# Optimization experiments

Measured on AMD Instinct MI355X. Metric: run time of the kernel, lower is better.

The kernel has to match this reference:

```python
import jax, jax.numpy as jnp
import numpy as np

H_PARAM = 3.0   # filtering strength h
TWS = 5         # template window size
SWS = 11        # search window size


def _shift_stack(x, window_size):
    # [N,C,H,W] -> [N,C,H,W,window_size**2] of circularly shifted copies.
    # Shift order matches the torch module: outer loop x_shift, inner y_shift,
    # roll shifts=(y_shift, x_shift) on dims (H, W).
    r = window_size // 2
    return jnp.stack(
        [jnp.roll(x, (ys, xs), axis=(2, 3))
         for xs in range(-r, r + 1) for ys in range(-r, r + 1)],
        axis=-1,
    )


def _box_filter(x, window_size):
    # Circular box-sum over H,W dims. The torch double roll loop is separable,
    # so do it as two 1-D roll sums (10 rolls instead of 25 for tws=5).
    r = window_size // 2
    s = x
    acc = x
    for k in range(1, r + 1):
        acc = acc + jnp.roll(s, k, axis=3) + jnp.roll(s, -k, axis=3)
    s2 = acc
    for k in range(1, r + 1):
        acc = acc + jnp.roll(s2, k, axis=2) + jnp.roll(s2, -k, axis=2)
    return acc


def setup_inputs() -> dict:
    key = jax.random.key(0)
    x = jax.random.uniform(key, (2, 3, 512, 512), dtype=jnp.float32)
    return {"x": x}


def reference(x):
    # luminance (RGB input: C == 3)
    xc = jnp.clip(x, 0.0, 1.0)
    y = 0.299 * xc[:, :1] + 0.587 * xc[:, 1:2] + 0.114 * xc[:, 2:3]  # [N,1,H,W]

    x_stack = _shift_stack(x, SWS)  # [N,3,H,W,sws^2]
    y_stack = _shift_stack(y, SWS)  # [N,1,H,W,sws^2]

    d2 = _box_filter((y[..., None] - y_stack) ** 2, TWS)  # [N,1,H,W,sws^2]
    distances = jnp.sqrt(d2)
    weights = jnp.exp(-distances / H_PARAM)                # [N,1,H,W,sws^2]

    denoised = (weights * x_stack).sum(axis=-1) / weights.sum(axis=-1)
    return jnp.clip(denoised, 0.0, 1.0)
```

## Files before the change

### kernel.cpp

```cpp
#include <hip/hip_runtime.h>
#include <math.h>


#define H_IMG 512
#define W_IMG 512
#define MASK  511
#define HWSZ  (H_IMG * W_IMG)
#define TILE  32
#define HALO  7
#define XD    46
#define YSTR  48
#define HSTR  44
#define VSTR  44

typedef _Float16 h2 __attribute__((ext_vector_type(2)));

__device__ __forceinline__ float fdot2(h2 a, h2 b, float c) {
#if __has_builtin(__builtin_amdgcn_fdot2)
    return __builtin_amdgcn_fdot2(a, b, c, false);
#else
    return c + (float)a.x * (float)b.x + (float)a.y * (float)b.y;
#endif
}

__device__ __forceinline__ float fast_exp2(float x) {
#if __has_builtin(__builtin_amdgcn_exp2f)
    return __builtin_amdgcn_exp2f(x);
#else
    return __expf(x * 0.6931471805599453f);
#endif
}

#define K2C   0.23126321070979063f
#define N2K2 -0.46252642141958126f

__global__ __launch_bounds__(256, 4)
void nlm_kernel(const float* __restrict__ x, float* __restrict__ out) {
    __shared__ float4   ldsX[XD * XD];
    __shared__ float    ldsYf[XD * YSTR];
    __shared__ unsigned ldsY2[XD * YSTR];
    __shared__ float    ldsH[XD * HSTR];
    __shared__ float    ldsV[42 * VSTR];

    const int n  = blockIdx.z;
    const int ti = blockIdx.y * TILE;
    const int tj = blockIdx.x * TILE;
    const int tx = threadIdx.x;
    const int ty = threadIdx.y;
    const int tid = ty * 32 + tx;

    const float* xb = x + (size_t)n * 3 * HWSZ;

    for (int e = tid; e < XD * XD; e += 256) {
        int r = e / XD, c = e - r * XD;
        int gi = (ti + r - HALO) & MASK;
        int gj = (tj + c - HALO) & MASK;
        size_t o = (size_t)gi * W_IMG + gj;
        ldsX[e] = make_float4(xb[o], xb[o + HWSZ], xb[o + 2 * HWSZ], 0.f);
    }
    __syncthreads();

    for (int e = tid; e < XD * 47; e += 256) {
        int r = e / 47, c = e - r * 47;
        int cs = (c == 46) ? 45 : c;
        float4 v = ldsX[r * XD + cs];
        float rr = fminf(fmaxf(v.x, 0.f), 1.f);
        float gg = fminf(fmaxf(v.y, 0.f), 1.f);
        float bb = fminf(fmaxf(v.z, 0.f), 1.f);
        ldsYf[r * YSTR + c] = 0.299f * rr + 0.587f * gg + 0.114f * bb;
    }
    __syncthreads();

    for (int e = tid; e < XD * XD; e += 256) {
        int r = e / XD, c = e - r * XD;
        h2 p;
        p.x = (_Float16)ldsYf[r * YSTR + c];
        p.y = (_Float16)ldsYf[r * YSTR + c + 1];
        ldsY2[r * YSTR + c] = __builtin_bit_cast(unsigned, p);
    }
    __syncthreads();

    for (int e = tid; e < XD * 42; e += 256) {
        int r = e / 42, c = e - r * 42;
        h2 a  = __builtin_bit_cast(h2, ldsY2[r * YSTR + c]);
        h2 b  = __builtin_bit_cast(h2, ldsY2[r * YSTR + c + 2]);
        h2 cc = __builtin_bit_cast(h2, ldsY2[r * YSTR + c + 4]);
        float x0 = (float)a.x, x1 = (float)a.y;
        float x2 = (float)b.x, x3 = (float)b.y;
        float x4 = (float)cc.x;
        ldsH[r * HSTR + c] = x0*x0 + x1*x1 + x2*x2 + x3*x3 + x4*x4;
    }
    __syncthreads();

    for (int e = tid; e < 42 * 42; e += 256) {
        int r = e / 42, c = e - r * 42;
        const float* hp = &ldsH[r * HSTR + c];
        float s = ((hp[0] + hp[HSTR]) + (hp[2*HSTR] + hp[3*HSTR])) + hp[4*HSTR];
        ldsV[r * VSTR + c] = K2C * s;
    }
    __syncthreads();

    const int jl = tx + HALO;
    const int il = ty * 4 + HALO;

    h2 cyP[8][3];
    float Vc[4];
    {
        float hcv[8];
        #pragma unroll
        for (int t = 0; t < 8; ++t) {
            int base = (il - 2 + t) * YSTR + (jl - 2);
            cyP[t][0] = __builtin_bit_cast(h2, ldsY2[base]);
            cyP[t][1] = __builtin_bit_cast(h2, ldsY2[base + 2]);
            h2 z = __builtin_bit_cast(h2, ldsY2[base + 4]);
            z.y = (_Float16)0.f;
            cyP[t][2] = z;
            hcv[t] = ldsH[(il - 2 + t) * HSTR + (jl - 2)];
        }
        float v0 = ((hcv[0] + hcv[1]) + (hcv[2] + hcv[3])) + hcv[4];
        float v1 = v0 - hcv[0] + hcv[5];
        float v2 = v1 - hcv[1] + hcv[6];
        float v3 = v2 - hcv[2] + hcv[7];
        Vc[0] = K2C * v0; Vc[1] = K2C * v1; Vc[2] = K2C * v2; Vc[3] = K2C * v3;
    }

    float den[4]  = {0.f, 0.f, 0.f, 0.f};
    float num0[4] = {0.f, 0.f, 0.f, 0.f};
    float num1[4] = {0.f, 0.f, 0.f, 0.f};
    float num2[4] = {0.f, 0.f, 0.f, 0.f};

    #pragma unroll 1
    for (int xs = -5; xs <= 5; ++xs) {
        const int jc  = jl - xs - 2;
        const int xjc = jl - xs;

        h2     swP[8][3];
        float  Wr[4];
        float4 xw[4];

        #pragma unroll
        for (int t = 0; t < 8; ++t) {
            int base = (il - 7 + t) * YSTR + jc;
            swP[t][0] = __builtin_bit_cast(h2, ldsY2[base]);
            swP[t][1] = __builtin_bit_cast(h2, ldsY2[base + 2]);
            swP[t][2] = __builtin_bit_cast(h2, ldsY2[base + 4]);
        }
        #pragma unroll
        for (int t = 0; t < 4; ++t) {
            Wr[t] = ldsV[(il - 7 + t) * VSTR + jc];
            xw[t] = ldsX[(il - 5 + t) * XD + xjc];
        }

        #pragma unroll
        for (int k = 0; k <= 10; ++k) {
            h2 nsw0, nsw1, nsw2; float nWv; float4 nxw;
            if (k < 10) {
                const int nr = il + k + 1;
                int base = nr * YSTR + jc;
                nsw0 = __builtin_bit_cast(h2, ldsY2[base]);
                nsw1 = __builtin_bit_cast(h2, ldsY2[base + 2]);
                nsw2 = __builtin_bit_cast(h2, ldsY2[base + 4]);
                nWv  = ldsV[(il + k - 3) * VSTR + jc];
                nxw  = ldsX[(il + k - 1) * XD + xjc];
            }

            float s[8];
            #pragma unroll
            for (int t = 0; t < 8; ++t) {
                const int m = (t + k) & 7;
                s[t] = fdot2(cyP[t][0], swP[m][0],
                       fdot2(cyP[t][1], swP[m][1],
                       fdot2(cyP[t][2], swP[m][2], 0.f)));
            }

            float S0 = ((s[0] + s[1]) + (s[2] + s[3])) + s[4];
            float S1 = S0 - s[0] + s[5];
            float S2 = S1 - s[1] + s[6];
            float S3 = S2 - s[2] + s[7];

            float d2a[4];
            d2a[0] = fmaf(N2K2, S0, Vc[0] + Wr[k & 3]);
            d2a[1] = fmaf(N2K2, S1, Vc[1] + Wr[(k + 1) & 3]);
            d2a[2] = fmaf(N2K2, S2, Vc[2] + Wr[(k + 2) & 3]);
            d2a[3] = fmaf(N2K2, S3, Vc[3] + Wr[(k + 3) & 3]);

            #pragma unroll
            for (int o = 0; o < 4; ++o) {
                float sd = __builtin_amdgcn_sqrtf(__builtin_fabsf(d2a[o]));
                float w  = fast_exp2(-sd);
                float4 xv = xw[(k + o) & 3];
                num0[o] = fmaf(w, xv.x, num0[o]);
                num1[o] = fmaf(w, xv.y, num1[o]);
                num2[o] = fmaf(w, xv.z, num2[o]);
                den[o] += w;
            }

            if (k < 10) {
                swP[k & 7][0] = nsw0;
                swP[k & 7][1] = nsw1;
                swP[k & 7][2] = nsw2;
                Wr[k & 3] = nWv;
                xw[k & 3] = nxw;
            }
        }
    }

    float* ob = out + (size_t)n * 3 * HWSZ;
    #pragma unroll
    for (int o = 0; o < 4; ++o) {
        int gi = ti + ty * 4 + o;
        int gj = tj + tx;
        size_t off = (size_t)gi * W_IMG + gj;
        float inv = __builtin_amdgcn_rcpf(den[o]);
        float v0 = fminf(fmaxf(num0[o] * inv, 0.f), 1.f);
        float v1 = fminf(fmaxf(num1[o] * inv, 0.f), 1.f);
        float v2 = fminf(fmaxf(num2[o] * inv, 0.f), 1.f);
        ob[off]            = v0;
        ob[off + HWSZ]     = v1;
        ob[off + 2 * HWSZ] = v2;
    }
}

extern "C" void kernel_launch(void* const* d_in, const int* in_sizes, int n_in,
                              void* d_out, int out_size, void* d_ws, size_t ws_size,
                              hipStream_t stream) {
    const float* x = (const float*)d_in[0];
    float* out = (float*)d_out;
    dim3 grid(W_IMG / TILE, H_IMG / TILE, 2);
    dim3 block(32, 8);
    nlm_kernel<<<grid, block, 0, stream>>>(x, out);
}
```

Measured before the change: 98.98 us.

## Split search-window columns across two thread halves and reduce through LDS

Doubles the block to 512 threads; each half handles part of the horizontal search offsets (6 and 5 columns) for the same output pixels, and the partial sums are combined through shared memory before the final normalization. The centre-pixel V terms are now read from the precomputed ldsV instead of recomputed from ldsH. This aims to double the wavefronts per block to hide latency during the preamble and main loop. The cost is an extra LDS reduction with two barriers, uneven work between the halves, and possibly higher register pressure under the 512-thread launch bound.

```diff
diff --git a/kernel.cpp b/kernel.cpp
--- a/kernel.cpp
+++ b/kernel.cpp
@@ -12,6 +12,7 @@
 #define YSTR  48
 #define HSTR  44
 #define VSTR  44
+#define NTHR  512
 
 typedef _Float16 h2 __attribute__((ext_vector_type(2)));
 
@@ -34,7 +35,7 @@
 #define K2C   0.23126321070979063f
 #define N2K2 -0.46252642141958126f
 
-__global__ __launch_bounds__(256, 4)
+__global__ __launch_bounds__(NTHR, 4)
 void nlm_kernel(const float* __restrict__ x, float* __restrict__ out) {
     __shared__ float4   ldsX[XD * XD];
     __shared__ float    ldsYf[XD * YSTR];
@@ -48,10 +49,12 @@
     const int tx = threadIdx.x;
     const int ty = threadIdx.y;
     const int tid = ty * 32 + tx;
+    const int ry = ty & 7;
+    const int hf = ty >> 3;
 
     const float* xb = x + (size_t)n * 3 * HWSZ;
 
-    for (int e = tid; e < XD * XD; e += 256) {
+    for (int e = tid; e < XD * XD; e += NTHR) {
         int r = e / XD, c = e - r * XD;
         int gi = (ti + r - HALO) & MASK;
         int gj = (tj + c - HALO) & MASK;
@@ -60,7 +63,7 @@
     }
     __syncthreads();
 
-    for (int e = tid; e < XD * 47; e += 256) {
+    for (int e = tid; e < XD * 47; e += NTHR) {
         int r = e / 47, c = e - r * 47;
         int cs = (c == 46) ? 45 : c;
         float4 v = ldsX[r * XD + cs];
@@ -71,7 +74,7 @@
     }
     __syncthreads();
 
-    for (int e = tid; e < XD * XD; e += 256) {
+    for (int e = tid; e < XD * XD; e += NTHR) {
         int r = e / XD, c = e - r * XD;
         h2 p;
         p.x = (_Float16)ldsYf[r * YSTR + c];
@@ -80,7 +83,7 @@
     }
     __syncthreads();
 
-    for (int e = tid; e < XD * 42; e += 256) {
+    for (int e = tid; e < XD * 42; e += NTHR) {
         int r = e / 42, c = e - r * 42;
         h2 a  = __builtin_bit_cast(h2, ldsY2[r * YSTR + c]);
         h2 b  = __builtin_bit_cast(h2, ldsY2[r * YSTR + c + 2]);
@@ -92,7 +95,7 @@
     }
     __syncthreads();
 
-    for (int e = tid; e < 42 * 42; e += 256) {
+    for (int e = tid; e < 42 * 42; e += NTHR) {
         int r = e / 42, c = e - r * 42;
         const float* hp = &ldsH[r * HSTR + c];
         float s = ((hp[0] + hp[HSTR]) + (hp[2*HSTR] + hp[3*HSTR])) + hp[4*HSTR];
@@ -101,36 +104,33 @@
     __syncthreads();
 
     const int jl = tx + HALO;
-    const int il = ty * 4 + HALO;
+    const int il = ry * 4 + HALO;
 
     h2 cyP[8][3];
     float Vc[4];
-    {
-        float hcv[8];
-        #pragma unroll
-        for (int t = 0; t < 8; ++t) {
-            int base = (il - 2 + t) * YSTR + (jl - 2);
-            cyP[t][0] = __builtin_bit_cast(h2, ldsY2[base]);
-            cyP[t][1] = __builtin_bit_cast(h2, ldsY2[base + 2]);
-            h2 z = __builtin_bit_cast(h2, ldsY2[base + 4]);
-            z.y = (_Float16)0.f;
-            cyP[t][2] = z;
-            hcv[t] = ldsH[(il - 2 + t) * HSTR + (jl - 2)];
-        }
-        float v0 = ((hcv[0] + hcv[1]) + (hcv[2] + hcv[3])) + hcv[4];
-        float v1 = v0 - hcv[0] + hcv[5];
-        float v2 = v1 - hcv[1] + hcv[6];
-        float v3 = v2 - hcv[2] + hcv[7];
-        Vc[0] = K2C * v0; Vc[1] = K2C * v1; Vc[2] = K2C * v2; Vc[3] = K2C * v3;
-    }
-
-    float den[4]  = {0.f, 0.f, 0.f, 0.f};
+    #pragma unroll
+    for (int t = 0; t < 8; ++t) {
+        int base = (il - 2 + t) * YSTR + (jl - 2);
+        cyP[t][0] = __builtin_bit_cast(h2, ldsY2[base]);
+        cyP[t][1] = __builtin_bit_cast(h2, ldsY2[base + 2]);
+        h2 z = __builtin_bit_cast(h2, ldsY2[base + 4]);
+        z.y = (_Float16)0.f;
+        cyP[t][2] = z;
+    }
+    #pragma unroll
+    for (int o = 0; o < 4; ++o)
+        Vc[o] = ldsV[(il - 2 + o) * VSTR + (jl - 2)];
+
     float num0[4] = {0.f, 0.f, 0.f, 0.f};
     float num1[4] = {0.f, 0.f, 0.f, 0.f};
     float num2[4] = {0.f, 0.f, 0.f, 0.f};
+    float den[4]  = {0.f, 0.f, 0.f, 0.f};
+
+    const int xsBeg = hf ? 1 : -5;
+    const int xsEnd = hf ? 5 : 0;
 
     #pragma unroll 1
-    for (int xs = -5; xs <= 5; ++xs) {
+    for (int xs = xsBeg; xs <= xsEnd; ++xs) {
         const int jc  = jl - xs - 2;
         const int xjc = jl - xs;
 
@@ -205,19 +205,35 @@
         }
     }
 
-    float* ob = out + (size_t)n * 3 * HWSZ;
-    #pragma unroll
-    for (int o = 0; o < 4; ++o) {
-        int gi = ti + ty * 4 + o;
-        int gj = tj + tx;
-        size_t off = (size_t)gi * W_IMG + gj;
-        float inv = __builtin_amdgcn_rcpf(den[o]);
-        float v0 = fminf(fmaxf(num0[o] * inv, 0.f), 1.f);
-        float v1 = fminf(fmaxf(num1[o] * inv, 0.f), 1.f);
-        float v2 = fminf(fmaxf(num2[o] * inv, 0.f), 1.f);
-        ob[off]            = v0;
-        ob[off + HWSZ]     = v1;
-        ob[off + 2 * HWSZ] = v2;
+    __syncthreads();
+    if (hf == 1) {
+        #pragma unroll
+        for (int o = 0; o < 4; ++o)
+            ldsX[(ry * 4 + o) * TILE + tx] =
+                make_float4(num0[o], num1[o], num2[o], den[o]);
+    }
+    __syncthreads();
+
+    if (hf == 0) {
+        float* ob = out + (size_t)n * 3 * HWSZ;
+        #pragma unroll
+        for (int o = 0; o < 4; ++o) {
+            float4 p = ldsX[(ry * 4 + o) * TILE + tx];
+            float nn0 = num0[o] + p.x;
+            float nn1 = num1[o] + p.y;
+            float nn2 = num2[o] + p.z;
+            float dd  = den[o]  + p.w;
+            int gi = ti + ry * 4 + o;
+            int gj = tj + tx;
+            size_t off = (size_t)gi * W_IMG + gj;
+            float inv = __builtin_amdgcn_rcpf(dd);
+            float v0 = fminf(fmaxf(nn0 * inv, 0.f), 1.f);
+            float v1 = fminf(fmaxf(nn1 * inv, 0.f), 1.f);
+            float v2 = fminf(fmaxf(nn2 * inv, 0.f), 1.f);
+            ob[off]            = v0;
+            ob[off + HWSZ]     = v1;
+            ob[off + 2 * HWSZ] = v2;
+        }
     }
 }
 
@@ -227,6 +243,6 @@
     const float* x = (const float*)d_in[0];
     float* out = (float*)d_out;
     dim3 grid(W_IMG / TILE, H_IMG / TILE, 2);
-    dim3 block(32, 8);
+    dim3 block(32, 16);
     nlm_kernel<<<grid, block, 0, stream>>>(x, out);
 }
```

After: 146.8 us. 1.48x slower.
